# Performance work log

Hardware: AMD Instinct MI355X
Metric: run time of the kernel (lower is better)

Reference implementation:

```python
import jax, jax.numpy as jnp
import numpy as np

D_MODEL = 1024
N_HEADS = 16
D_HIDDEN = 4096
BATCH = 2
N_CTX = 2048


def setup_inputs() -> dict:
    key = jax.random.key(0)
    ks = jax.random.split(key, 4)
    scale = 0.02
    x = jax.random.normal(ks[0], (BATCH, N_CTX, D_MODEL), dtype=jnp.float32)
    Wk = jax.random.normal(ks[1], (D_MODEL, D_MODEL), dtype=jnp.float32) * scale
    bk = jnp.zeros((D_MODEL,), dtype=jnp.float32)
    Wv = jax.random.normal(ks[2], (D_MODEL, D_HIDDEN), dtype=jnp.float32) * scale
    bv = jnp.zeros((D_HIDDEN,), dtype=jnp.float32)
    Wf = jax.random.normal(ks[3], (D_HIDDEN, D_MODEL), dtype=jnp.float32) * scale
    bf = jnp.zeros((D_MODEL,), dtype=jnp.float32)
    return {"x": x, "Wk": Wk, "bk": bk, "Wv": Wv, "bv": bv, "Wf": Wf, "bf": bf}


def _split_heads(t, n_heads):
    # [..., S, D] -> [..., H, S, D/H]
    B, S, D = t.shape
    return t.reshape(B, S, n_heads, D // n_heads).transpose(0, 2, 1, 3)


def reference(x, Wk, bk, Wv, bv, Wf, bf):
    B, S, D = x.shape
    H = N_HEADS
    # Q is raw x split into heads (no query projection in this module)
    Q = _split_heads(x, H)                  # [B,H,S,dk]
    K = _split_heads(x @ Wk + bk, H)        # [B,H,S,dk]
    V = _split_heads(x @ Wv + bv, H)        # [B,H,S,dv]
    # additive causal mask: 0 on/below diagonal, -inf strictly above
    causal = jnp.tril(jnp.ones((S, S), dtype=bool))
    mask = jnp.where(causal, 0.0, -jnp.inf).astype(x.dtype)
    # NOTE: no 1/sqrt(d) scaling, faithful to the original
    scores = jnp.einsum("bhqd,bhkd->bhqk", Q, K) + mask
    attn = jax.nn.softmax(scores, axis=-1)
    o = jnp.einsum("bhqk,bhkd->bhqd", attn, V)   # [B,H,S,dv]
    o = o.transpose(0, 2, 1, 3).reshape(B, S, -1)  # [B,S,d_hidden]
    return x + jax.nn.gelu(o, approximate=False) @ Wf + bf
```

## Files before the change

### kernel.cpp

```cpp
#include <hip/hip_runtime.h>
#include <math.h>

typedef unsigned short u16;
typedef __attribute__((ext_vector_type(8))) short bf16x8;
typedef __attribute__((ext_vector_type(4))) float f32x4;

__device__ __forceinline__ float b2f(u16 u) {
    union { unsigned int i; float f; } v; v.i = ((unsigned int)u) << 16; return v.f;
}
__device__ __forceinline__ u16 f2b(float f) {
    union { float f; unsigned int i; } v; v.f = f;
    unsigned int r = v.i + 0x7FFFu + ((v.i >> 16) & 1u);
    return (u16)(r >> 16);
}
__device__ __forceinline__ float gelu_exact(float v) {
    return 0.5f * v * (1.0f + erff(v * 0.70710678118654752f));
}

__device__ __forceinline__ void load_lds16(const u16* gp, u16* lp) {
    __builtin_amdgcn_global_load_lds(
        (const __attribute__((address_space(1))) void*)gp,
        (__attribute__((address_space(3))) void*)lp,
        16, 0, 0);
}

__global__ __launch_bounds__(256) void convert_f2b(const float* __restrict__ in,
                                                   u16* __restrict__ out) {
    const int idx = blockIdx.x * 256 + threadIdx.x;
    float4 v = ((const float4*)in)[idx];
    ushort4 u; u.x = f2b(v.x); u.y = f2b(v.y); u.z = f2b(v.z); u.w = f2b(v.w);
    ((ushort4*)out)[idx] = u;
}

__global__ __launch_bounds__(256) void transpose_w(const float* __restrict__ W,
                                                   u16* __restrict__ Wt, int N, int K) {
    __shared__ float t[32][33];
    const int tid = threadIdx.x;
    const int k0 = blockIdx.y * 32, n0 = blockIdx.x * 32;
    const int c = tid & 31, r = tid >> 5;
    #pragma unroll
    for (int p = 0; p < 4; p++)
        t[r + p * 8][c] = W[(size_t)(k0 + r + p * 8) * N + n0 + c];
    __syncthreads();
    #pragma unroll
    for (int p = 0; p < 4; p++)
        Wt[(size_t)(n0 + r + p * 8) * K + k0 + c] = f2b(t[c][r + p * 8]);
}

template <int EPI>
__global__ __launch_bounds__(256) void mfma_gemm(
    const u16* __restrict__ A, const u16* __restrict__ Bt,
    const float* __restrict__ bias, const float* __restrict__ resid,
    void* __restrict__ Cv, int M, int N, int K)
{
    __shared__ u16 As[64 * 64];
    __shared__ u16 Bs[128 * 64];

    const int tid = threadIdx.x;
    const int w = tid >> 6, lane = tid & 63;
    const int m16 = lane & 15, quad = lane >> 4;
    const int wm = w >> 1, wn = w & 1;
    const int row0 = blockIdx.y * 64, col0 = blockIdx.x * 128;
    const int lr = lane >> 3, lc = lane & 7;
    const int sw8 = (lc ^ (lr & 7)) * 8;

    f32x4 acc[2][4];
    #pragma unroll
    for (int i = 0; i < 2; i++)
        #pragma unroll
        for (int j = 0; j < 4; j++) acc[i][j] = (f32x4){0.f, 0.f, 0.f, 0.f};

    for (int k0 = 0; k0 < K; k0 += 64) {
        __syncthreads();
        #pragma unroll
        for (int c2 = 0; c2 < 2; c2++)
            load_lds16(A + (size_t)(row0 + c2 * 32 + w * 8 + lr) * K + k0 + sw8,
                       &As[(c2 * 32 + w * 8) * 64]);
        #pragma unroll
        for (int c2 = 0; c2 < 4; c2++)
            load_lds16(Bt + (size_t)(col0 + c2 * 32 + w * 8 + lr) * K + k0 + sw8,
                       &Bs[(c2 * 32 + w * 8) * 64]);
        __syncthreads();

        bf16x8 af[2][2], bfr[4][2];
        #pragma unroll
        for (int mt = 0; mt < 2; mt++)
            #pragma unroll
            for (int ks = 0; ks < 2; ks++)
                af[mt][ks] = *(const bf16x8*)&As[(wm * 32 + mt * 16 + m16) * 64 +
                                                 (((ks * 4 + quad) ^ (m16 & 7)) * 8)];
        #pragma unroll
        for (int nt = 0; nt < 4; nt++)
            #pragma unroll
            for (int ks = 0; ks < 2; ks++)
                bfr[nt][ks] = *(const bf16x8*)&Bs[(wn * 64 + nt * 16 + m16) * 64 +
                                                  (((ks * 4 + quad) ^ (m16 & 7)) * 8)];

        #pragma unroll
        for (int ks = 0; ks < 2; ks++)
            #pragma unroll
            for (int mt = 0; mt < 2; mt++)
                #pragma unroll
                for (int nt = 0; nt < 4; nt++)
                    acc[mt][nt] = __builtin_amdgcn_mfma_f32_16x16x32_bf16(af[mt][ks], bfr[nt][ks], acc[mt][nt], 0, 0, 0);
    }

    #pragma unroll
    for (int mt = 0; mt < 2; mt++) {
        #pragma unroll
        for (int nt = 0; nt < 4; nt++) {
            const int c = col0 + wn * 64 + nt * 16 + m16;
            const float bc = bias[c];
            #pragma unroll
            for (int reg = 0; reg < 4; reg++) {
                const int r = row0 + wm * 32 + mt * 16 + quad * 4 + reg;
                float v = acc[mt][nt][reg] + bc;
                if (EPI == 1) {
                    v += resid[(size_t)r * N + c];
                    ((float*)Cv)[(size_t)r * N + c] = v;
                } else {
                    ((u16*)Cv)[(size_t)r * N + c] = f2b(v);
                }
            }
        }
    }
}

__global__ __launch_bounds__(256) void mfma_gemm128_tv(
    const u16* __restrict__ A, const u16* __restrict__ Bt,
    const float* __restrict__ bias,
    u16* __restrict__ Cv, int M, int N, int K)
{
    __shared__ u16 As[128 * 64];
    __shared__ u16 Bs[128 * 64];

    const int tid = threadIdx.x;
    const int w = tid >> 6, lane = tid & 63;
    const int m16 = lane & 15, quad = lane >> 4;
    const int wm = w >> 1, wn = w & 1;
    const int row0 = blockIdx.y * 128, col0 = blockIdx.x * 128;
    const int lr = lane >> 3, lc = lane & 7;
    const int sw8 = (lc ^ (lr & 7)) * 8;

    f32x4 acc[4][4];
    #pragma unroll
    for (int i = 0; i < 4; i++)
        #pragma unroll
        for (int j = 0; j < 4; j++) acc[i][j] = (f32x4){0.f, 0.f, 0.f, 0.f};

    for (int k0 = 0; k0 < K; k0 += 64) {
        __syncthreads();
        #pragma unroll
        for (int c2 = 0; c2 < 4; c2++)
            load_lds16(A + (size_t)(row0 + c2 * 32 + w * 8 + lr) * K + k0 + sw8,
                       &As[(c2 * 32 + w * 8) * 64]);
        #pragma unroll
        for (int c2 = 0; c2 < 4; c2++)
            load_lds16(Bt + (size_t)(col0 + c2 * 32 + w * 8 + lr) * K + k0 + sw8,
                       &Bs[(c2 * 32 + w * 8) * 64]);
        __syncthreads();

        bf16x8 af[4][2], bfr[4][2];
        #pragma unroll
        for (int mt = 0; mt < 4; mt++)
            #pragma unroll
            for (int ks = 0; ks < 2; ks++)
                af[mt][ks] = *(const bf16x8*)&As[(wm * 64 + mt * 16 + m16) * 64 +
                                                 (((ks * 4 + quad) ^ (m16 & 7)) * 8)];
        #pragma unroll
        for (int nt = 0; nt < 4; nt++)
            #pragma unroll
            for (int ks = 0; ks < 2; ks++)
                bfr[nt][ks] = *(const bf16x8*)&Bs[(wn * 64 + nt * 16 + m16) * 64 +
                                                  (((ks * 4 + quad) ^ (m16 & 7)) * 8)];

        #pragma unroll
        for (int ks = 0; ks < 2; ks++)
            #pragma unroll
            for (int mt = 0; mt < 4; mt++)
                #pragma unroll
                for (int nt = 0; nt < 4; nt++)
                    acc[mt][nt] = __builtin_amdgcn_mfma_f32_16x16x32_bf16(af[mt][ks], bfr[nt][ks], acc[mt][nt], 0, 0, 0);
    }

    #pragma unroll
    for (int mt = 0; mt < 4; mt++) {
        const int r0 = row0 + wm * 64 + mt * 16 + quad * 4;
        const int bb = r0 >> 11, s = r0 & 2047;
        #pragma unroll
        for (int nt = 0; nt < 4; nt++) {
            const int c = col0 + wn * 64 + nt * 16 + m16;
            const int h = c >> 8, dv = c & 255;
            const float bc = bias[c];
            ushort4 w4;
            w4.x = f2b(acc[mt][nt][0] + bc);
            w4.y = f2b(acc[mt][nt][1] + bc);
            w4.z = f2b(acc[mt][nt][2] + bc);
            w4.w = f2b(acc[mt][nt][3] + bc);
            *(ushort4*)(Cv + (((size_t)((bb * 16 + h) * 256 + dv)) << 11) + s) = w4;
        }
    }
}

__global__ __launch_bounds__(256) void attn_kernel(
    const float* __restrict__ X,
    const u16*  __restrict__ Kb,
    const u16*  __restrict__ Vt,
    u16* __restrict__ O,
    int B, int S)
{
    const int DM = 1024, DH = 4096;
    __shared__ u16 Ks[64 * 64];
    __shared__ u16 Ps[64 * 64];

    const int tid = threadIdx.x;
    const int w = tid >> 6, lane = tid & 63;
    const int m16 = lane & 15, quad = lane >> 4;
    const int lr = lane >> 3, lc = lane & 7;
    const int sw8 = (lc ^ (lr & 7)) * 8;
    const int b = blockIdx.z, h = blockIdx.y;
    const int qt = (S / 64 - 1) - blockIdx.x;
    const int q0 = qt * 64;
    const size_t baseRow = (size_t)b * S;
    const size_t vhead = ((size_t)(b * 16 + h) * 256) << 11;

    bf16x8 aq[2];
    {
        const float* qsrc = X + (baseRow + q0 + w * 16 + m16) * DM + h * 64;
        #pragma unroll
        for (int ks = 0; ks < 2; ks++) {
            float4 v0 = *(const float4*)(qsrc + ks * 32 + quad * 8);
            float4 v1 = *(const float4*)(qsrc + ks * 32 + quad * 8 + 4);
            bf16x8 u;
            u[0] = (short)f2b(v0.x); u[1] = (short)f2b(v0.y); u[2] = (short)f2b(v0.z); u[3] = (short)f2b(v0.w);
            u[4] = (short)f2b(v1.x); u[5] = (short)f2b(v1.y); u[6] = (short)f2b(v1.z); u[7] = (short)f2b(v1.w);
            aq[ks] = u;
        }
    }

    f32x4 o_acc[4][4];
    #pragma unroll
    for (int i = 0; i < 4; i++)
        #pragma unroll
        for (int j = 0; j < 4; j++) o_acc[i][j] = (f32x4){0.f, 0.f, 0.f, 0.f};
    f32x4 lacc4[4];
    #pragma unroll
    for (int i = 0; i < 4; i++) lacc4[i] = (f32x4){0.f, 0.f, 0.f, 0.f};

    bf16x8 onesf;
    {
        const short one = (m16 == 0) ? (short)0x3F80 : (short)0;
        #pragma unroll
        for (int i = 0; i < 8; i++) onesf[i] = one;
    }

    bf16x8 kreg[2], vreg[4][2];
    const int nch = qt + 1;

    #pragma unroll
    for (int p = 0; p < 2; p++)
        kreg[p] = *(const bf16x8*)(Kb + (baseRow + p * 32 + w * 8 + lr) * DM + h * 64 + sw8);
    #pragma unroll
    for (int nt2 = 0; nt2 < 4; nt2++)
        #pragma unroll
        for (int ks = 0; ks < 2; ks++)
            vreg[nt2][ks] = *(const bf16x8*)(Vt + vhead +
                (((size_t)(w * 64 + nt2 * 16 + m16)) << 11) + ks * 32 + quad * 8);
    #pragma unroll
    for (int p = 0; p < 2; p++)
        *(bf16x8*)&Ks[(p * 32 + w * 8) * 64 + lane * 8] = kreg[p];
    if (nch > 1) {
        #pragma unroll
        for (int p = 0; p < 2; p++)
            kreg[p] = *(const bf16x8*)(Kb + (baseRow + 64 + p * 32 + w * 8 + lr) * DM + h * 64 + sw8);
    }
    __syncthreads();

    for (int ch = 0; ch < nch; ch++) {
        const int k0 = ch * 64;

        const int qg = q0 + w * 16 + quad * 4;
        #pragma unroll
        for (int nt = 0; nt < 4; nt++) {
            f32x4 acc = (f32x4){0.f, 0.f, 0.f, 0.f};
            #pragma unroll
            for (int ks = 0; ks < 2; ks++) {
                bf16x8 bk8 = *(const bf16x8*)&Ks[(nt * 16 + m16) * 64 + (((ks * 4 + quad) ^ (m16 & 7)) * 8)];
                acc = __builtin_amdgcn_mfma_f32_16x16x32_bf16(aq[ks], bk8, acc, 0, 0, 0);
            }
            const int kg = k0 + nt * 16 + m16;
            #pragma unroll
            for (int reg = 0; reg < 4; reg++) {
                const float p = (kg <= qg + reg) ? __expf(acc[reg] - 20.f) : 0.f;
                const int srow = w * 16 + quad * 4 + reg;
                Ps[srow * 64 + (((nt * 2 + (m16 >> 3)) ^ (srow & 7)) * 8) + (m16 & 7)] = f2b(p);
            }
        }
        __syncthreads();

        if (ch + 1 < nch) {
            #pragma unroll
            for (int p = 0; p < 2; p++)
                *(bf16x8*)&Ks[(p * 32 + w * 8) * 64 + lane * 8] = kreg[p];
            if (ch + 2 < nch) {
                #pragma unroll
                for (int p = 0; p < 2; p++)
                    kreg[p] = *(const bf16x8*)(Kb + (baseRow + k0 + 128 + p * 32 + w * 8 + lr) * DM + h * 64 + sw8);
            }
        }

        #pragma unroll
        for (int mt = 0; mt < 4; mt++) {
            bf16x8 pa0 = *(const bf16x8*)&Ps[(mt * 16 + m16) * 64 + (((0 + quad) ^ (m16 & 7)) * 8)];
            bf16x8 pa1 = *(const bf16x8*)&Ps[(mt * 16 + m16) * 64 + (((4 + quad) ^ (m16 & 7)) * 8)];
            lacc4[mt] = __builtin_amdgcn_mfma_f32_16x16x32_bf16(pa0, onesf, lacc4[mt], 0, 0, 0);
            lacc4[mt] = __builtin_amdgcn_mfma_f32_16x16x32_bf16(pa1, onesf, lacc4[mt], 0, 0, 0);
            #pragma unroll
            for (int nt2 = 0; nt2 < 4; nt2++) {
                f32x4 acc = o_acc[mt][nt2];
                acc = __builtin_amdgcn_mfma_f32_16x16x32_bf16(pa0, vreg[nt2][0], acc, 0, 0, 0);
                acc = __builtin_amdgcn_mfma_f32_16x16x32_bf16(pa1, vreg[nt2][1], acc, 0, 0, 0);
                o_acc[mt][nt2] = acc;
            }
        }

        if (ch + 1 < nch) {
            #pragma unroll
            for (int nt2 = 0; nt2 < 4; nt2++)
                #pragma unroll
                for (int ks = 0; ks < 2; ks++)
                    vreg[nt2][ks] = *(const bf16x8*)(Vt + vhead +
                        (((size_t)(w * 64 + nt2 * 16 + m16)) << 11) + (k0 + 64) + ks * 32 + quad * 8);
        }
        __syncthreads();
    }

    #pragma unroll
    for (int mt = 0; mt < 4; mt++) {
        #pragma unroll
        for (int reg = 0; reg < 4; reg++) {
            const float l = __shfl(lacc4[mt][reg], quad * 16);
            const float invl = 1.0f / l;
            u16* orow = O + (baseRow + q0 + mt * 16 + quad * 4 + reg) * DH + h * 256 + w * 64 + m16;
            #pragma unroll
            for (int nt2 = 0; nt2 < 4; nt2++)
                orow[nt2 * 16] = f2b(gelu_exact(o_acc[mt][nt2][reg] * invl));
        }
    }
}

extern "C" void kernel_launch(void* const* d_in, const int* in_sizes, int n_in,
                              void* d_out, int out_size, void* d_ws, size_t ws_size,
                              hipStream_t stream)
{
    const float* x   = (const float*)d_in[0];
    const float* Wk  = (const float*)d_in[1];
    const float* bk  = (const float*)d_in[2];
    const float* Wv  = (const float*)d_in[3];
    const float* bv  = (const float*)d_in[4];
    const float* Wf  = (const float*)d_in[5];
    const float* bfb = (const float*)d_in[6];
    float* out = (float*)d_out;

    const int Bsz = 2, S = 2048, DM = 1024, DH = 4096;
    const int M = Bsz * S;
    const size_t MB = 1024 * 1024;

    u16* xb   = (u16*)d_ws;
    u16* Wkt  = xb   + 4 * MB;
    u16* Wvt  = Wkt  + 1 * MB;
    u16* Wft  = Wvt  + 4 * MB;
    u16* Kbuf = Wft  + 4 * MB;
    u16* Vt   = Kbuf + 4 * MB;
    u16* Obuf = Vt   + 16 * MB;

    dim3 blk(256);

    convert_f2b<<<dim3(M * DM / 1024), blk, 0, stream>>>(x, xb);
    transpose_w<<<dim3(DM / 32, DM / 32), blk, 0, stream>>>(Wk, Wkt, DM, DM);
    transpose_w<<<dim3(DH / 32, DM / 32), blk, 0, stream>>>(Wv, Wvt, DH, DM);
    transpose_w<<<dim3(DM / 32, DH / 32), blk, 0, stream>>>(Wf, Wft, DM, DH);

    mfma_gemm<0><<<dim3(DM / 128, M / 64), blk, 0, stream>>>(xb, Wkt, bk, nullptr, Kbuf, M, DM, DM);
    mfma_gemm128_tv<<<dim3(DH / 128, M / 128), blk, 0, stream>>>(xb, Wvt, bv, Vt, M, DH, DM);
    attn_kernel<<<dim3(S / 64, 16, Bsz), blk, 0, stream>>>(x, Kbuf, Vt, Obuf, Bsz, S);
    mfma_gemm<1><<<dim3(DM / 128, M / 64), blk, 0, stream>>>(Obuf, Wft, bfb, x, out, M, DM, DH);
}
```

Measured before the change: 400.9 us.

## Pair causal query tiles per block and stage V tiles in LDS

```diff
diff --git a/kernel.cpp b/kernel.cpp
--- a/kernel.cpp
+++ b/kernel.cpp
@@ -211,41 +211,48 @@
 {
     const int DM = 1024, DH = 4096;
     __shared__ u16 Ks[64 * 64];
-    __shared__ u16 Ps[64 * 64];
+    __shared__ u16 PsA[64 * 64];
+    __shared__ u16 PsB[64 * 64];
+    __shared__ u16 Vts[256 * 64];
 
     const int tid = threadIdx.x;
     const int w = tid >> 6, lane = tid & 63;
     const int m16 = lane & 15, quad = lane >> 4;
     const int lr = lane >> 3, lc = lane & 7;
     const int sw8 = (lc ^ (lr & 7)) * 8;
-    const int b = blockIdx.z, h = blockIdx.y;
-    const int qt = (S / 64 - 1) - blockIdx.x;
-    const int q0 = qt * 64;
+    const int b = blockIdx.z, h = blockIdx.y, bx = blockIdx.x;
+    const int NT = S / 64;
+    const int qtA = (NT - 1) - bx;
+    const int qtB = bx;
+    const int q0A = qtA * 64, q0B = qtB * 64;
+    const int nchA = qtA + 1, nchB = qtB + 1;
     const size_t baseRow = (size_t)b * S;
     const size_t vhead = ((size_t)(b * 16 + h) * 256) << 11;
 
-    bf16x8 aq[2];
+    bf16x8 aqA[2], aqB[2];
     {
-        const float* qsrc = X + (baseRow + q0 + w * 16 + m16) * DM + h * 64;
+        const float* qA = X + (baseRow + q0A + w * 16 + m16) * DM + h * 64;
+        const float* qB = X + (baseRow + q0B + w * 16 + m16) * DM + h * 64;
         #pragma unroll
         for (int ks = 0; ks < 2; ks++) {
-            float4 v0 = *(const float4*)(qsrc + ks * 32 + quad * 8);
-            float4 v1 = *(const float4*)(qsrc + ks * 32 + quad * 8 + 4);
-            bf16x8 u;
-            u[0] = (short)f2b(v0.x); u[1] = (short)f2b(v0.y); u[2] = (short)f2b(v0.z); u[3] = (short)f2b(v0.w);
-            u[4] = (short)f2b(v1.x); u[5] = (short)f2b(v1.y); u[6] = (short)f2b(v1.z); u[7] = (short)f2b(v1.w);
-            aq[ks] = u;
-        }
-    }
-
-    f32x4 o_acc[4][4];
-    #pragma unroll
-    for (int i = 0; i < 4; i++)
-        #pragma unroll
-        for (int j = 0; j < 4; j++) o_acc[i][j] = (f32x4){0.f, 0.f, 0.f, 0.f};
-    f32x4 lacc4[4];
-    #pragma unroll
-    for (int i = 0; i < 4; i++) lacc4[i] = (f32x4){0.f, 0.f, 0.f, 0.f};
+            float4 a0 = *(const float4*)(qA + ks * 32 + quad * 8);
+            float4 a1 = *(const float4*)(qA + ks * 32 + quad * 8 + 4);
+            float4 b0 = *(const float4*)(qB + ks * 32 + quad * 8);
+            float4 b1 = *(const float4*)(qB + ks * 32 + quad * 8 + 4);
+            bf16x8 ua, ub;
+            ua[0] = (short)f2b(a0.x); ua[1] = (short)f2b(a0.y); ua[2] = (short)f2b(a0.z); ua[3] = (short)f2b(a0.w);
+            ua[4] = (short)f2b(a1.x); ua[5] = (short)f2b(a1.y); ua[6] = (short)f2b(a1.z); ua[7] = (short)f2b(a1.w);
+            ub[0] = (short)f2b(b0.x); ub[1] = (short)f2b(b0.y); ub[2] = (short)f2b(b0.z); ub[3] = (short)f2b(b0.w);
+            ub[4] = (short)f2b(b1.x); ub[5] = (short)f2b(b1.y); ub[6] = (short)f2b(b1.z); ub[7] = (short)f2b(b1.w);
+            aqA[ks] = ua; aqB[ks] = ub;
+        }
+    }
+
+    f32x4 oA[16], oB[16];
+    #pragma unroll
+    for (int i = 0; i < 16; i++) { oA[i] = (f32x4){0.f, 0.f, 0.f, 0.f}; oB[i] = (f32x4){0.f, 0.f, 0.f, 0.f}; }
+    f32x4 laccA = (f32x4){0.f, 0.f, 0.f, 0.f};
+    f32x4 laccB = (f32x4){0.f, 0.f, 0.f, 0.f};
 
     bf16x8 onesf;
     {
@@ -254,97 +261,114 @@
         for (int i = 0; i < 8; i++) onesf[i] = one;
     }
 
-    bf16x8 kreg[2], vreg[4][2];
-    const int nch = qt + 1;
-
+    bf16x8 kreg[2], vreg[8];
     #pragma unroll
     for (int p = 0; p < 2; p++)
         kreg[p] = *(const bf16x8*)(Kb + (baseRow + p * 32 + w * 8 + lr) * DM + h * 64 + sw8);
     #pragma unroll
-    for (int nt2 = 0; nt2 < 4; nt2++)
-        #pragma unroll
-        for (int ks = 0; ks < 2; ks++)
-            vreg[nt2][ks] = *(const bf16x8*)(Vt + vhead +
-                (((size_t)(w * 64 + nt2 * 16 + m16)) << 11) + ks * 32 + quad * 8);
+    for (int p = 0; p < 8; p++)
+        vreg[p] = *(const bf16x8*)(Vt + vhead + (((size_t)(p * 32 + w * 8 + lr)) << 11) + sw8);
     #pragma unroll
     for (int p = 0; p < 2; p++)
         *(bf16x8*)&Ks[(p * 32 + w * 8) * 64 + lane * 8] = kreg[p];
-    if (nch > 1) {
-        #pragma unroll
-        for (int p = 0; p < 2; p++)
-            kreg[p] = *(const bf16x8*)(Kb + (baseRow + 64 + p * 32 + w * 8 + lr) * DM + h * 64 + sw8);
-    }
+    #pragma unroll
+    for (int p = 0; p < 8; p++)
+        *(bf16x8*)&Vts[(p * 32 + w * 8) * 64 + lane * 8] = vreg[p];
     __syncthreads();
 
-    for (int ch = 0; ch < nch; ch++) {
+    for (int ch = 0; ch < nchA; ch++) {
         const int k0 = ch * 64;
-
-        const int qg = q0 + w * 16 + quad * 4;
+        const bool doB = (ch < nchB);
+
+        if (ch + 1 < nchA) {
+            const int kn = k0 + 64;
+            #pragma unroll
+            for (int p = 0; p < 2; p++)
+                kreg[p] = *(const bf16x8*)(Kb + (baseRow + kn + p * 32 + w * 8 + lr) * DM + h * 64 + sw8);
+            #pragma unroll
+            for (int p = 0; p < 8; p++)
+                vreg[p] = *(const bf16x8*)(Vt + vhead + (((size_t)(p * 32 + w * 8 + lr)) << 11) + kn + sw8);
+        }
+
+        f32x4 sA[4], sB[4];
         #pragma unroll
         for (int nt = 0; nt < 4; nt++) {
-            f32x4 acc = (f32x4){0.f, 0.f, 0.f, 0.f};
+            sA[nt] = (f32x4){0.f, 0.f, 0.f, 0.f};
+            sB[nt] = (f32x4){0.f, 0.f, 0.f, 0.f};
             #pragma unroll
             for (int ks = 0; ks < 2; ks++) {
                 bf16x8 bk8 = *(const bf16x8*)&Ks[(nt * 16 + m16) * 64 + (((ks * 4 + quad) ^ (m16 & 7)) * 8)];
-                acc = __builtin_amdgcn_mfma_f32_16x16x32_bf16(aq[ks], bk8, acc, 0, 0, 0);
+                sA[nt] = __builtin_amdgcn_mfma_f32_16x16x32_bf16(aqA[ks], bk8, sA[nt], 0, 0, 0);
+                if (doB)
+                    sB[nt] = __builtin_amdgcn_mfma_f32_16x16x32_bf16(aqB[ks], bk8, sB[nt], 0, 0, 0);
             }
+        }
+
+        const int qgA = q0A + w * 16 + quad * 4;
+        const int qgB = q0B + w * 16 + quad * 4;
+        #pragma unroll
+        for (int nt = 0; nt < 4; nt++) {
             const int kg = k0 + nt * 16 + m16;
             #pragma unroll
             for (int reg = 0; reg < 4; reg++) {
-                const float p = (kg <= qg + reg) ? __expf(acc[reg] - 20.f) : 0.f;
                 const int srow = w * 16 + quad * 4 + reg;
-                Ps[srow * 64 + (((nt * 2 + (m16 >> 3)) ^ (srow & 7)) * 8) + (m16 & 7)] = f2b(p);
+                const int scol = (((nt * 2 + (m16 >> 3)) ^ (srow & 7)) * 8) + (m16 & 7);
+                const float pA = (kg <= qgA + reg) ? __expf(sA[nt][reg] - 20.f) : 0.f;
+                PsA[srow * 64 + scol] = f2b(pA);
+                if (doB) {
+                    const float pB = (kg <= qgB + reg) ? __expf(sB[nt][reg] - 20.f) : 0.f;
+                    PsB[srow * 64 + scol] = f2b(pB);
+                }
             }
         }
+
+        bf16x8 paA[2], paB[2];
+        #pragma unroll
+        for (int ks = 0; ks < 2; ks++) {
+            const int off = (w * 16 + m16) * 64 + (((ks * 4 + quad) ^ (m16 & 7)) * 8);
+            paA[ks] = *(const bf16x8*)&PsA[off];
+            laccA = __builtin_amdgcn_mfma_f32_16x16x32_bf16(paA[ks], onesf, laccA, 0, 0, 0);
+            if (doB) {
+                paB[ks] = *(const bf16x8*)&PsB[off];
+                laccB = __builtin_amdgcn_mfma_f32_16x16x32_bf16(paB[ks], onesf, laccB, 0, 0, 0);
+            }
+        }
+
+        #pragma unroll
+        for (int nt2 = 0; nt2 < 16; nt2++) {
+            #pragma unroll
+            for (int ks = 0; ks < 2; ks++) {
+                bf16x8 bv8 = *(const bf16x8*)&Vts[(nt2 * 16 + m16) * 64 + (((ks * 4 + quad) ^ (m16 & 7)) * 8)];
+                oA[nt2] = __builtin_amdgcn_mfma_f32_16x16x32_bf16(paA[ks], bv8, oA[nt2], 0, 0, 0);
+                if (doB)
+                    oB[nt2] = __builtin_amdgcn_mfma_f32_16x16x32_bf16(paB[ks], bv8, oB[nt2], 0, 0, 0);
+            }
+        }
+
         __syncthreads();
-
-        if (ch + 1 < nch) {
+        if (ch + 1 < nchA) {
             #pragma unroll
             for (int p = 0; p < 2; p++)
                 *(bf16x8*)&Ks[(p * 32 + w * 8) * 64 + lane * 8] = kreg[p];
-            if (ch + 2 < nch) {
-                #pragma unroll
-                for (int p = 0; p < 2; p++)
-                    kreg[p] = *(const bf16x8*)(Kb + (baseRow + k0 + 128 + p * 32 + w * 8 + lr) * DM + h * 64 + sw8);
-            }
-        }
-
-        #pragma unroll
-        for (int mt = 0; mt < 4; mt++) {
-            bf16x8 pa0 = *(const bf16x8*)&Ps[(mt * 16 + m16) * 64 + (((0 + quad) ^ (m16 & 7)) * 8)];
-            bf16x8 pa1 = *(const bf16x8*)&Ps[(mt * 16 + m16) * 64 + (((4 + quad) ^ (m16 & 7)) * 8)];
-            lacc4[mt] = __builtin_amdgcn_mfma_f32_16x16x32_bf16(pa0, onesf, lacc4[mt], 0, 0, 0);
-            lacc4[mt] = __builtin_amdgcn_mfma_f32_16x16x32_bf16(pa1, onesf, lacc4[mt], 0, 0, 0);
-            #pragma unroll
-            for (int nt2 = 0; nt2 < 4; nt2++) {
-                f32x4 acc = o_acc[mt][nt2];
-                acc = __builtin_amdgcn_mfma_f32_16x16x32_bf16(pa0, vreg[nt2][0], acc, 0, 0, 0);
-                acc = __builtin_amdgcn_mfma_f32_16x16x32_bf16(pa1, vreg[nt2][1], acc, 0, 0, 0);
-                o_acc[mt][nt2] = acc;
-            }
-        }
-
-        if (ch + 1 < nch) {
-            #pragma unroll
-            for (int nt2 = 0; nt2 < 4; nt2++)
-                #pragma unroll
-                for (int ks = 0; ks < 2; ks++)
-                    vreg[nt2][ks] = *(const bf16x8*)(Vt + vhead +
-                        (((size_t)(w * 64 + nt2 * 16 + m16)) << 11) + (k0 + 64) + ks * 32 + quad * 8);
-        }
-        __syncthreads();
-    }
-
-    #pragma unroll
-    for (int mt = 0; mt < 4; mt++) {
-        #pragma unroll
-        for (int reg = 0; reg < 4; reg++) {
-            const float l = __shfl(lacc4[mt][reg], quad * 16);
-            const float invl = 1.0f / l;
-            u16* orow = O + (baseRow + q0 + mt * 16 + quad * 4 + reg) * DH + h * 256 + w * 64 + m16;
-            #pragma unroll
-            for (int nt2 = 0; nt2 < 4; nt2++)
-                orow[nt2 * 16] = f2b(gelu_exact(o_acc[mt][nt2][reg] * invl));
+            #pragma unroll
+            for (int p = 0; p < 8; p++)
+                *(bf16x8*)&Vts[(p * 32 + w * 8) * 64 + lane * 8] = vreg[p];
+            __syncthreads();
+        }
+    }
+
+    #pragma unroll
+    for (int reg = 0; reg < 4; reg++) {
+        const float lA = __shfl(laccA[reg], quad * 16);
+        const float lB = __shfl(laccB[reg], quad * 16);
+        const float invA = 1.0f / lA;
+        const float invB = 1.0f / lB;
+        u16* orowA = O + (baseRow + q0A + w * 16 + quad * 4 + reg) * DH + h * 256 + m16;
+        u16* orowB = O + (baseRow + q0B + w * 16 + quad * 4 + reg) * DH + h * 256 + m16;
+        #pragma unroll
+        for (int nt2 = 0; nt2 < 16; nt2++) {
+            orowA[nt2 * 16] = f2b(gelu_exact(oA[nt2][reg] * invA));
+            orowB[nt2 * 16] = f2b(gelu_exact(oB[nt2][reg] * invB));
         }
     }
 }
@@ -383,6 +407,6 @@
 
     mfma_gemm<0><<<dim3(DM / 128, M / 64), blk, 0, stream>>>(xb, Wkt, bk, nullptr, Kbuf, M, DM, DM);
     mfma_gemm128_tv<<<dim3(DH / 128, M / 128), blk, 0, stream>>>(xb, Wvt, bv, Vt, M, DH, DM);
-    attn_kernel<<<dim3(S / 64, 16, Bsz), blk, 0, stream>>>(x, Kbuf, Vt, Obuf, Bsz, S);
+    attn_kernel<<<dim3(S / 128, 16, Bsz), blk, 0, stream>>>(x, Kbuf, Vt, Obuf, Bsz, S);
     mfma_gemm<1><<<dim3(DM / 128, M / 64), blk, 0, stream>>>(Obuf, Wft, bfb, x, out, M, DM, DH);
 }
```

After: 448.3 us. 1.12x slower.

## Stage V tiles through swizzled LDS with coalesced one-chunk-ahead prefetch

Applied to the files above, without the earlier changes.

```diff
diff --git a/kernel.cpp b/kernel.cpp
--- a/kernel.cpp
+++ b/kernel.cpp
@@ -212,6 +212,7 @@
     const int DM = 1024, DH = 4096;
     __shared__ u16 Ks[64 * 64];
     __shared__ u16 Ps[64 * 64];
+    __shared__ u16 Vts[256 * 64];
 
     const int tid = threadIdx.x;
     const int w = tid >> 6, lane = tid & 63;
@@ -254,30 +255,35 @@
         for (int i = 0; i < 8; i++) onesf[i] = one;
     }
 
-    bf16x8 kreg[2], vreg[4][2];
-    const int nch = qt + 1;
-
+    bf16x8 kreg[2], vreg[8];
     #pragma unroll
     for (int p = 0; p < 2; p++)
         kreg[p] = *(const bf16x8*)(Kb + (baseRow + p * 32 + w * 8 + lr) * DM + h * 64 + sw8);
     #pragma unroll
-    for (int nt2 = 0; nt2 < 4; nt2++)
-        #pragma unroll
-        for (int ks = 0; ks < 2; ks++)
-            vreg[nt2][ks] = *(const bf16x8*)(Vt + vhead +
-                (((size_t)(w * 64 + nt2 * 16 + m16)) << 11) + ks * 32 + quad * 8);
+    for (int p = 0; p < 8; p++)
+        vreg[p] = *(const bf16x8*)(Vt + vhead + (((size_t)(p * 32 + w * 8 + lr)) << 11) + sw8);
     #pragma unroll
     for (int p = 0; p < 2; p++)
         *(bf16x8*)&Ks[(p * 32 + w * 8) * 64 + lane * 8] = kreg[p];
-    if (nch > 1) {
-        #pragma unroll
-        for (int p = 0; p < 2; p++)
-            kreg[p] = *(const bf16x8*)(Kb + (baseRow + 64 + p * 32 + w * 8 + lr) * DM + h * 64 + sw8);
-    }
+    #pragma unroll
+    for (int p = 0; p < 8; p++)
+        *(bf16x8*)&Vts[(p * 32 + w * 8) * 64 + lane * 8] = vreg[p];
     __syncthreads();
 
+    const int nch = qt + 1;
     for (int ch = 0; ch < nch; ch++) {
         const int k0 = ch * 64;
+        const bool more = (ch + 1 < nch);
+
+        if (more) {
+            const int kn = k0 + 64;
+            #pragma unroll
+            for (int p = 0; p < 2; p++)
+                kreg[p] = *(const bf16x8*)(Kb + (baseRow + kn + p * 32 + w * 8 + lr) * DM + h * 64 + sw8);
+            #pragma unroll
+            for (int p = 0; p < 8; p++)
+                vreg[p] = *(const bf16x8*)(Vt + vhead + (((size_t)(p * 32 + w * 8 + lr)) << 11) + kn + sw8);
+        }
 
         const int qg = q0 + w * 16 + quad * 4;
         #pragma unroll
@@ -298,15 +304,10 @@
         }
         __syncthreads();
 
-        if (ch + 1 < nch) {
+        if (more) {
             #pragma unroll
             for (int p = 0; p < 2; p++)
                 *(bf16x8*)&Ks[(p * 32 + w * 8) * 64 + lane * 8] = kreg[p];
-            if (ch + 2 < nch) {
-                #pragma unroll
-                for (int p = 0; p < 2; p++)
-                    kreg[p] = *(const bf16x8*)(Kb + (baseRow + k0 + 128 + p * 32 + w * 8 + lr) * DM + h * 64 + sw8);
-            }
         }
 
         #pragma unroll
@@ -317,22 +318,22 @@
             lacc4[mt] = __builtin_amdgcn_mfma_f32_16x16x32_bf16(pa1, onesf, lacc4[mt], 0, 0, 0);
             #pragma unroll
             for (int nt2 = 0; nt2 < 4; nt2++) {
+                const int vrow = w * 64 + nt2 * 16 + m16;
+                bf16x8 bv0 = *(const bf16x8*)&Vts[vrow * 64 + (((0 + quad) ^ (m16 & 7)) * 8)];
+                bf16x8 bv1 = *(const bf16x8*)&Vts[vrow * 64 + (((4 + quad) ^ (m16 & 7)) * 8)];
                 f32x4 acc = o_acc[mt][nt2];
-                acc = __builtin_amdgcn_mfma_f32_16x16x32_bf16(pa0, vreg[nt2][0], acc, 0, 0, 0);
-                acc = __builtin_amdgcn_mfma_f32_16x16x32_bf16(pa1, vreg[nt2][1], acc, 0, 0, 0);
+                acc = __builtin_amdgcn_mfma_f32_16x16x32_bf16(pa0, bv0, acc, 0, 0, 0);
+                acc = __builtin_amdgcn_mfma_f32_16x16x32_bf16(pa1, bv1, acc, 0, 0, 0);
                 o_acc[mt][nt2] = acc;
             }
         }
-
-        if (ch + 1 < nch) {
-            #pragma unroll
-            for (int nt2 = 0; nt2 < 4; nt2++)
-                #pragma unroll
-                for (int ks = 0; ks < 2; ks++)
-                    vreg[nt2][ks] = *(const bf16x8*)(Vt + vhead +
-                        (((size_t)(w * 64 + nt2 * 16 + m16)) << 11) + (k0 + 64) + ks * 32 + quad * 8);
-        }
-        __syncthreads();
+        __syncthreads();
+
+        if (more) {
+            #pragma unroll
+            for (int p = 0; p < 8; p++)
+                *(bf16x8*)&Vts[(p * 32 + w * 8) * 64 + lane * 8] = vreg[p];
+        }
     }
 
     #pragma unroll
```

Result: faster. 387.1 us (-3.4%).
